# Performance work log

Hardware: AMD Instinct MI355X
Metric: run time of the kernel (lower is better)

Reference implementation:

```python
import math
import jax, jax.numpy as jnp
import numpy as np

R = 15  # static Gaussian truncation radius (covers 3*sigma for resolutions up to ~12)
SIG_PER_FWHM = 1.0 / math.sqrt(8.0 * math.log(2.0))  # sigma = fwhm / sqrt(8 ln 2)


def _blur_resample_axis0(img, sigma, res):
    """Gaussian blur (dct2/symmetric boundary) + down/up resize along axis 0.

    img: [H, W]; sigma, res: scalars. anchor='f' resize convention:
      down (factor=1/res): low coord j samples input at j*res
      up   (factor=res, shape=H): out coord i samples low grid at i/res
    Low-res grid has n_low = max(floor(H/res), 1) valid rows; positions are
    clamped to the valid range (edge boundary).
    """
    H, W = img.shape
    dt = img.dtype
    # --- separable 1D Gaussian blur along axis 0 ---
    off = jnp.arange(-R, R + 1, dtype=dt)
    sig = jnp.maximum(sigma, jnp.asarray(1e-6, dt))
    w = jnp.exp(-0.5 * (off / sig) ** 2)
    w = w / w.sum()
    pad = jnp.pad(img, ((R, R), (0, 0)), mode='symmetric')  # dct2 boundary
    s = w[0] * pad[0:H]
    for k in range(1, 2 * R + 1):
        s = s + w[k] * pad[k:k + H]
    # --- downsample (factor = 1/res, anchor 'f') ---
    Hf = jnp.asarray(H, dt)
    n_low = jnp.maximum(jnp.floor(Hf / res), 1.0).astype(jnp.int32)
    pos = jnp.clip(jnp.arange(H, dtype=dt) * res, 0.0, Hf - 1.0)
    lo = jnp.floor(pos)
    fr = (pos - lo)[:, None]
    lo_i = lo.astype(jnp.int32)
    hi_i = jnp.minimum(lo_i + 1, H - 1)
    low = s[lo_i] * (1.0 - fr) + s[hi_i] * fr  # [H, W], rows >= n_low unused
    # --- upsample back to H (factor = res, anchor 'f') ---
    pos2 = jnp.clip(jnp.arange(H, dtype=dt) / res, 0.0, n_low.astype(dt) - 1.0)
    lo2 = jnp.floor(pos2)
    fr2 = (pos2 - lo2)[:, None]
    lo2_i = jnp.minimum(lo2.astype(jnp.int32), n_low - 1)
    hi2_i = jnp.minimum(lo2_i + 1, n_low - 1)
    return low[lo2_i] * (1.0 - fr2) + low[hi2_i] * fr2


def _process_one(img, res, ax, gp):
    fwhm = res * gp
    sigma = fwhm * SIG_PER_FWHM
    out0 = _blur_resample_axis0(img, sigma, res)          # degrade axis 0 (H)
    out1 = _blur_resample_axis0(img.T, sigma, res).T      # degrade axis 1 (W)
    return jnp.where(ax == 0, out0, out1)


def setup_inputs() -> dict:
    key = jax.random.key(0)
    k_x, k_res, k_ax, k_gap = jax.random.split(key, 4)
    B, C, H, W = 16, 4, 512, 512
    x = jax.random.normal(k_x, (B, C, H, W), dtype=jnp.float32)
    # lognormal with mean 3, sd 3 -> underlying normal params
    m, sdev = 3.0, 3.0
    var_log = math.log(1.0 + (sdev / m) ** 2)
    mu = math.log(m) - 0.5 * var_log
    z = jax.random.normal(k_res, (B, C), dtype=jnp.float32)
    resolution = jnp.clip(jnp.exp(mu + math.sqrt(var_log) * z), 1.0, None)
    axis = jax.random.randint(k_ax, (B, C), 0, 2, dtype=jnp.int32)
    gap = jax.random.uniform(k_gap, (B, C), dtype=jnp.float32)
    return {"x": x, "resolution": resolution, "axis": axis, "gap": gap}


def reference(x, resolution, axis, gap):
    B, C, H, W = x.shape
    flat = x.reshape(B * C, H, W)
    out = jax.vmap(_process_one)(flat, resolution.reshape(-1), axis.reshape(-1), gap.reshape(-1))
    return out.reshape(B, C, H, W)
```

## Files before the change

### kernel.cpp

```cpp
#include <hip/hip_runtime.h>
#include <math.h>


#define RR 15
#define TAPS 31
#define SIG_PER_FWHM 0.42466090014400953f
#define SW(t) ((t) ^ (((t) >> 3) & 7))

__global__ __launch_bounds__(256) void lowres2d_kernel(
    const float* __restrict__ x,
    const float* __restrict__ resolution,
    const int*   __restrict__ axis,
    const float* __restrict__ gap,
    float* __restrict__ out)
{
    const int tid = threadIdx.x;
    const int n   = blockIdx.y;
    const int bx  = blockIdx.x;

    const float res = resolution[n];
    const int   ax  = axis[n];
    const float gp  = gap[n];

    if (ax == 0 && bx >= 64) return;

    const float sig = fmaxf(res * gp * SIG_PER_FWHM, 1e-6f);
    int n_low = (int)floorf(512.0f / res);
    if (n_low < 1) n_low = 1;
    if (n_low > 512) n_low = 512;
    const float nlm1f = (float)(n_low - 1);

    int kr = (int)(sig * 5.2565f) + 1;
    if (kr > RR) kr = RR;
    const int k0 = RR - kr, k1 = RR + 1 + kr;
    const int la_lo = kr, la_hi = 510 - kr;

    __shared__ float2 wd[32];
    __shared__ __align__(16) float smem[4608];
    float (*s_imgT)[4]   = (float (*)[4])smem;
    float (*s_lowT)[4]   = (float (*)[4])(smem + 2048);
    float (*s_lowB)[512] = (float (*)[512])smem;

    if (tid < 32) {
        const int k = tid;
        float r = 0.0f;
        if (k < TAPS) {
            float d = (float)(k - RR) / sig;
            r = expf(-0.5f * d * d);
        }
        float tot = r;
        tot += __shfl_xor(tot, 1, 32);
        tot += __shfl_xor(tot, 2, 32);
        tot += __shfl_xor(tot, 4, 32);
        tot += __shfl_xor(tot, 8, 32);
        tot += __shfl_xor(tot, 16, 32);
        float rm1 = __shfl_up(r, 1, 32);
        if (k == 0) rm1 = 0.0f;
        const float inv = 1.0f / tot;
        wd[k] = make_float2(r * inv, (rm1 - r) * inv);
    }
    __syncthreads();

    const size_t base = (size_t)n * (512 * 512);
    const float* img = x + base;
    float* o = out + base;

    if (ax == 0) {
        const int i0 = bx * 8;
        const int g  = tid >> 7;
        const int lt = tid & 127;
        const float4* img4 = (const float4*)img;
        float4* out4 = (float4*)o;

        float pA = fminf((float)i0 / res, nlm1f);
        int jlo = (int)floorf(pA);
        float pB = fminf((float)(i0 + 7) / res, nlm1f);
        int jhi = (int)floorf(pB) + 1;
        if (jhi > n_low - 1) jhi = n_low - 1;
        if (jhi < jlo) jhi = jlo;
        const int nrows = jhi - jlo + 1;

        for (int p = 0; p < nrows; p += 2) {
            int rowoff = p + g;
            int j = jlo + ((rowoff < nrows) ? rowoff : (nrows - 1));
            float pos = fminf((float)j * res, 511.0f);
            float lof = floorf(pos);
            float fr  = pos - lof;
            int   la  = __builtin_amdgcn_readfirstlane((int)lof);
            float4 acc = make_float4(0.0f, 0.0f, 0.0f, 0.0f);
            if (la >= la_lo && la <= la_hi) {
                #pragma unroll 4
                for (int k = k0; k <= k1; ++k) {
                    int t = la - RR + k;
                    float2 w = wd[k];
                    float cw = fmaf(fr, w.y, w.x);
                    float4 v = img4[(size_t)(t * 128 + lt)];
                    acc.x = fmaf(cw, v.x, acc.x);
                    acc.y = fmaf(cw, v.y, acc.y);
                    acc.z = fmaf(cw, v.z, acc.z);
                    acc.w = fmaf(cw, v.w, acc.w);
                }
            } else {
                for (int k = k0; k <= k1; ++k) {
                    int t = la - RR + k;
                    t = (t < 0)   ? (-1 - t)   : t;
                    t = (t > 511) ? (1023 - t) : t;
                    float2 w = wd[k];
                    float cw = fmaf(fr, w.y, w.x);
                    float4 v = img4[(size_t)(t * 128 + lt)];
                    acc.x = fmaf(cw, v.x, acc.x);
                    acc.y = fmaf(cw, v.y, acc.y);
                    acc.z = fmaf(cw, v.z, acc.z);
                    acc.w = fmaf(cw, v.w, acc.w);
                }
            }
            if (rowoff < nrows) {
                ((float4*)&s_lowB[rowoff][0])[lt] = acc;
            }
        }
        __syncthreads();

        #pragma unroll
        for (int p = 0; p < 4; ++p) {
            int i = i0 + p * 2 + g;
            float pos2 = fminf((float)i / res, nlm1f);
            float l2f  = floorf(pos2);
            float fr2  = pos2 - l2f;
            int lo2 = (int)l2f;
            int hi2 = (lo2 + 1 <= jhi) ? (lo2 + 1) : jhi;
            float4 A = ((float4*)&s_lowB[lo2 - jlo][0])[lt];
            float4 B = ((float4*)&s_lowB[hi2 - jlo][0])[lt];
            float omf2 = 1.0f - fr2;
            float4 ov;
            ov.x = A.x * omf2 + B.x * fr2;
            ov.y = A.y * omf2 + B.y * fr2;
            ov.z = A.z * omf2 + B.z * fr2;
            ov.w = A.w * omf2 + B.w * fr2;
            out4[(size_t)(i * 128 + lt)] = ov;
        }
    } else {
        const int h0 = bx * 4;
        const float* imgr = img + (size_t)h0 * 512;

        #pragma unroll
        for (int p = 0; p < 2; ++p) {
            int c = p * 256 + tid;
            float v0 = imgr[0 * 512 + c];
            float v1 = imgr[1 * 512 + c];
            float v2 = imgr[2 * 512 + c];
            float v3 = imgr[3 * 512 + c];
            *(float4*)&s_imgT[SW(c)][0] = make_float4(v0, v1, v2, v3);
        }
        __syncthreads();

        for (int j = tid; j < n_low; j += 256) {
            float pos = fminf((float)j * res, 511.0f);
            float lof = floorf(pos);
            float fr  = pos - lof;
            int   la  = (int)lof;
            float a0 = 0.0f, a1 = 0.0f, a2 = 0.0f, a3 = 0.0f;
            if (la >= la_lo && la <= la_hi) {
                #pragma unroll 4
                for (int k = k0; k <= k1; ++k) {
                    int t = la - RR + k;
                    float2 w = wd[k];
                    float cw = fmaf(fr, w.y, w.x);
                    float4 v = *(const float4*)&s_imgT[SW(t)][0];
                    a0 = fmaf(cw, v.x, a0);
                    a1 = fmaf(cw, v.y, a1);
                    a2 = fmaf(cw, v.z, a2);
                    a3 = fmaf(cw, v.w, a3);
                }
            } else {
                for (int k = k0; k <= k1; ++k) {
                    int t = la - RR + k;
                    t = (t < 0)   ? (-1 - t)   : t;
                    t = (t > 511) ? (1023 - t) : t;
                    float2 w = wd[k];
                    float cw = fmaf(fr, w.y, w.x);
                    float4 v = *(const float4*)&s_imgT[SW(t)][0];
                    a0 = fmaf(cw, v.x, a0);
                    a1 = fmaf(cw, v.y, a1);
                    a2 = fmaf(cw, v.z, a2);
                    a3 = fmaf(cw, v.w, a3);
                }
            }
            *(float4*)&s_lowT[SW(j)][0] = make_float4(a0, a1, a2, a3);
        }
        __syncthreads();

        {
            int ia = 2 * tid, ib = 2 * tid + 1;
            float posa = fminf((float)ia / res, nlm1f);
            float posb = fminf((float)ib / res, nlm1f);
            float lfa = floorf(posa), lfb = floorf(posb);
            float fra = posa - lfa,   frb = posb - lfb;
            int loa = (int)lfa, lob = (int)lfb;
            int hia = (loa + 1 < n_low) ? (loa + 1) : (n_low - 1);
            int hib = (lob + 1 < n_low) ? (lob + 1) : (n_low - 1);
            float oma = 1.0f - fra, omb = 1.0f - frb;
            float4 Aa = *(const float4*)&s_lowT[SW(loa)][0];
            float4 Ba = *(const float4*)&s_lowT[SW(hia)][0];
            float4 Ab = *(const float4*)&s_lowT[SW(lob)][0];
            float4 Bb = *(const float4*)&s_lowT[SW(hib)][0];
            #pragma unroll
            for (int r = 0; r < 4; ++r) {
                float va = (r == 0 ? Aa.x : r == 1 ? Aa.y : r == 2 ? Aa.z : Aa.w) * oma
                         + (r == 0 ? Ba.x : r == 1 ? Ba.y : r == 2 ? Ba.z : Ba.w) * fra;
                float vb = (r == 0 ? Ab.x : r == 1 ? Ab.y : r == 2 ? Ab.z : Ab.w) * omb
                         + (r == 0 ? Bb.x : r == 1 ? Bb.y : r == 2 ? Bb.z : Bb.w) * frb;
                ((float2*)(o + (size_t)(h0 + r) * 512))[tid] = make_float2(va, vb);
            }
        }
    }
}

extern "C" void kernel_launch(void* const* d_in, const int* in_sizes, int n_in,
                              void* d_out, int out_size, void* d_ws, size_t ws_size,
                              hipStream_t stream) {
    const float* x          = (const float*)d_in[0];
    const float* resolution = (const float*)d_in[1];
    const int*   axis       = (const int*)d_in[2];
    const float* gap        = (const float*)d_in[3];
    float* out = (float*)d_out;

    const int n_img = in_sizes[1];

    dim3 grid(128, n_img);
    lowres2d_kernel<<<grid, 256, 0, stream>>>(x, resolution, axis, gap, out);
}
```

Baseline: 125.6 us.

## Process eight rows per block on axis-1 path and use nontemporal stores

```diff
diff --git a/kernel.cpp b/kernel.cpp
--- a/kernel.cpp
+++ b/kernel.cpp
@@ -5,7 +5,10 @@
 #define RR 15
 #define TAPS 31
 #define SIG_PER_FWHM 0.42466090014400953f
-#define SW(t) ((t) ^ (((t) >> 3) & 7))
+#define SWB(b) ((b) ^ (((b) >> 3) & 7))
+
+typedef float f4v __attribute__((ext_vector_type(4)));
+typedef float f2v __attribute__((ext_vector_type(2)));
 
 __global__ __launch_bounds__(256) void lowres2d_kernel(
     const float* __restrict__ x,
@@ -22,8 +25,6 @@
     const int   ax  = axis[n];
     const float gp  = gap[n];
 
-    if (ax == 0 && bx >= 64) return;
-
     const float sig = fmaxf(res * gp * SIG_PER_FWHM, 1e-6f);
     int n_low = (int)floorf(512.0f / res);
     if (n_low < 1) n_low = 1;
@@ -36,9 +37,9 @@
     const int la_lo = kr, la_hi = 510 - kr;
 
     __shared__ float2 wd[32];
-    __shared__ __align__(16) float smem[4608];
+    __shared__ __align__(16) float smem[8192];
     float (*s_imgT)[4]   = (float (*)[4])smem;
-    float (*s_lowT)[4]   = (float (*)[4])(smem + 2048);
+    float (*s_lowT)[4]   = (float (*)[4])(smem + 4096);
     float (*s_lowB)[512] = (float (*)[512])smem;
 
     if (tid < 32) {
@@ -70,7 +71,6 @@
         const int g  = tid >> 7;
         const int lt = tid & 127;
         const float4* img4 = (const float4*)img;
-        float4* out4 = (float4*)o;
 
         float pA = fminf((float)i0 / res, nlm1f);
         int jlo = (int)floorf(pA);
@@ -131,15 +131,14 @@
             float4 A = ((float4*)&s_lowB[lo2 - jlo][0])[lt];
             float4 B = ((float4*)&s_lowB[hi2 - jlo][0])[lt];
             float omf2 = 1.0f - fr2;
-            float4 ov;
-            ov.x = A.x * omf2 + B.x * fr2;
-            ov.y = A.y * omf2 + B.y * fr2;
-            ov.z = A.z * omf2 + B.z * fr2;
-            ov.w = A.w * omf2 + B.w * fr2;
-            out4[(size_t)(i * 128 + lt)] = ov;
+            f4v ov = { A.x * omf2 + B.x * fr2,
+                       A.y * omf2 + B.y * fr2,
+                       A.z * omf2 + B.z * fr2,
+                       A.w * omf2 + B.w * fr2 };
+            __builtin_nontemporal_store(ov, (f4v*)o + (size_t)(i * 128 + lt));
         }
     } else {
-        const int h0 = bx * 4;
+        const int h0 = bx * 8;
         const float* imgr = img + (size_t)h0 * 512;
 
         #pragma unroll
@@ -149,7 +148,12 @@
             float v1 = imgr[1 * 512 + c];
             float v2 = imgr[2 * 512 + c];
             float v3 = imgr[3 * 512 + c];
-            *(float4*)&s_imgT[SW(c)][0] = make_float4(v0, v1, v2, v3);
+            float v4 = imgr[4 * 512 + c];
+            float v5 = imgr[5 * 512 + c];
+            float v6 = imgr[6 * 512 + c];
+            float v7 = imgr[7 * 512 + c];
+            *(float4*)&s_imgT[SWB(2 * c + 0)][0] = make_float4(v0, v1, v2, v3);
+            *(float4*)&s_imgT[SWB(2 * c + 1)][0] = make_float4(v4, v5, v6, v7);
         }
         __syncthreads();
 
@@ -158,18 +162,24 @@
             float lof = floorf(pos);
             float fr  = pos - lof;
             int   la  = (int)lof;
-            float a0 = 0.0f, a1 = 0.0f, a2 = 0.0f, a3 = 0.0f;
+            float a0 = 0.f, a1 = 0.f, a2 = 0.f, a3 = 0.f;
+            float a4 = 0.f, a5 = 0.f, a6 = 0.f, a7 = 0.f;
             if (la >= la_lo && la <= la_hi) {
                 #pragma unroll 4
                 for (int k = k0; k <= k1; ++k) {
                     int t = la - RR + k;
                     float2 w = wd[k];
                     float cw = fmaf(fr, w.y, w.x);
-                    float4 v = *(const float4*)&s_imgT[SW(t)][0];
-                    a0 = fmaf(cw, v.x, a0);
-                    a1 = fmaf(cw, v.y, a1);
-                    a2 = fmaf(cw, v.z, a2);
-                    a3 = fmaf(cw, v.w, a3);
+                    float4 u = *(const float4*)&s_imgT[SWB(2 * t + 0)][0];
+                    float4 v = *(const float4*)&s_imgT[SWB(2 * t + 1)][0];
+                    a0 = fmaf(cw, u.x, a0);
+                    a1 = fmaf(cw, u.y, a1);
+                    a2 = fmaf(cw, u.z, a2);
+                    a3 = fmaf(cw, u.w, a3);
+                    a4 = fmaf(cw, v.x, a4);
+                    a5 = fmaf(cw, v.y, a5);
+                    a6 = fmaf(cw, v.z, a6);
+                    a7 = fmaf(cw, v.w, a7);
                 }
             } else {
                 for (int k = k0; k <= k1; ++k) {
@@ -178,14 +188,20 @@
                     t = (t > 511) ? (1023 - t) : t;
                     float2 w = wd[k];
                     float cw = fmaf(fr, w.y, w.x);
-                    float4 v = *(const float4*)&s_imgT[SW(t)][0];
-                    a0 = fmaf(cw, v.x, a0);
-                    a1 = fmaf(cw, v.y, a1);
-                    a2 = fmaf(cw, v.z, a2);
-                    a3 = fmaf(cw, v.w, a3);
-                }
-            }
-            *(float4*)&s_lowT[SW(j)][0] = make_float4(a0, a1, a2, a3);
+                    float4 u = *(const float4*)&s_imgT[SWB(2 * t + 0)][0];
+                    float4 v = *(const float4*)&s_imgT[SWB(2 * t + 1)][0];
+                    a0 = fmaf(cw, u.x, a0);
+                    a1 = fmaf(cw, u.y, a1);
+                    a2 = fmaf(cw, u.z, a2);
+                    a3 = fmaf(cw, u.w, a3);
+                    a4 = fmaf(cw, v.x, a4);
+                    a5 = fmaf(cw, v.y, a5);
+                    a6 = fmaf(cw, v.z, a6);
+                    a7 = fmaf(cw, v.w, a7);
+                }
+            }
+            *(float4*)&s_lowT[SWB(2 * j + 0)][0] = make_float4(a0, a1, a2, a3);
+            *(float4*)&s_lowT[SWB(2 * j + 1)][0] = make_float4(a4, a5, a6, a7);
         }
         __syncthreads();
 
@@ -199,17 +215,25 @@
             int hia = (loa + 1 < n_low) ? (loa + 1) : (n_low - 1);
             int hib = (lob + 1 < n_low) ? (lob + 1) : (n_low - 1);
             float oma = 1.0f - fra, omb = 1.0f - frb;
-            float4 Aa = *(const float4*)&s_lowT[SW(loa)][0];
-            float4 Ba = *(const float4*)&s_lowT[SW(hia)][0];
-            float4 Ab = *(const float4*)&s_lowT[SW(lob)][0];
-            float4 Bb = *(const float4*)&s_lowT[SW(hib)][0];
+            float4 Aa0 = *(const float4*)&s_lowT[SWB(2 * loa + 0)][0];
+            float4 Aa1 = *(const float4*)&s_lowT[SWB(2 * loa + 1)][0];
+            float4 Ba0 = *(const float4*)&s_lowT[SWB(2 * hia + 0)][0];
+            float4 Ba1 = *(const float4*)&s_lowT[SWB(2 * hia + 1)][0];
+            float4 Ab0 = *(const float4*)&s_lowT[SWB(2 * lob + 0)][0];
+            float4 Ab1 = *(const float4*)&s_lowT[SWB(2 * lob + 1)][0];
+            float4 Bb0 = *(const float4*)&s_lowT[SWB(2 * hib + 0)][0];
+            float4 Bb1 = *(const float4*)&s_lowT[SWB(2 * hib + 1)][0];
+            float Aar[8] = {Aa0.x, Aa0.y, Aa0.z, Aa0.w, Aa1.x, Aa1.y, Aa1.z, Aa1.w};
+            float Bar[8] = {Ba0.x, Ba0.y, Ba0.z, Ba0.w, Ba1.x, Ba1.y, Ba1.z, Ba1.w};
+            float Abr[8] = {Ab0.x, Ab0.y, Ab0.z, Ab0.w, Ab1.x, Ab1.y, Ab1.z, Ab1.w};
+            float Bbr[8] = {Bb0.x, Bb0.y, Bb0.z, Bb0.w, Bb1.x, Bb1.y, Bb1.z, Bb1.w};
             #pragma unroll
-            for (int r = 0; r < 4; ++r) {
-                float va = (r == 0 ? Aa.x : r == 1 ? Aa.y : r == 2 ? Aa.z : Aa.w) * oma
-                         + (r == 0 ? Ba.x : r == 1 ? Ba.y : r == 2 ? Ba.z : Ba.w) * fra;
-                float vb = (r == 0 ? Ab.x : r == 1 ? Ab.y : r == 2 ? Ab.z : Ab.w) * omb
-                         + (r == 0 ? Bb.x : r == 1 ? Bb.y : r == 2 ? Bb.z : Bb.w) * frb;
-                ((float2*)(o + (size_t)(h0 + r) * 512))[tid] = make_float2(va, vb);
+            for (int r = 0; r < 8; ++r) {
+                float va = Aar[r] * oma + Bar[r] * fra;
+                float vb = Abr[r] * omb + Bbr[r] * frb;
+                f2v ov = { va, vb };
+                __builtin_nontemporal_store(
+                    ov, (f2v*)(o + (size_t)(h0 + r) * 512) + tid);
             }
         }
     }
@@ -226,6 +250,6 @@
 
     const int n_img = in_sizes[1];
 
-    dim3 grid(128, n_img);
+    dim3 grid(64, n_img);
     lowres2d_kernel<<<grid, 256, 0, stream>>>(x, resolution, axis, gap, out);
 }
```

Result: faster. 119.4 us, median of 2 (-4.9%).
